# Optimization experiments

Measured on AMD Instinct MI355X. Metric: run time of the kernel, lower is better.

Reference implementation:

```python
import jax, jax.numpy as jnp
import numpy as np

B, L, D = 32, 128, 512
Qn = 16          # n_querys
N, P = 512, 64   # gathered groups x group size


def setup_inputs() -> dict:
    key = jax.random.key(0)
    ks = jax.random.split(key, 10)
    s = 0.02
    return {
        "patch": jax.random.normal(ks[0], (B, L, D), jnp.float32),
        "query": jax.random.normal(ks[1], (1, Qn, D), jnp.float32),
        "Wk": jax.random.normal(ks[2], (D, D), jnp.float32) * s,
        "bk": jnp.zeros((D,), jnp.float32),
        "Wv": jax.random.normal(ks[3], (D, D), jnp.float32) * s,
        "bv": jnp.zeros((D,), jnp.float32),
        "Wf": jax.random.normal(ks[4], (D, 1), jnp.float32) * s,
        "bf": jnp.zeros((1,), jnp.float32),
        "indices": jax.random.randint(ks[5], (N, P), 0, B * L),
        "pos_mask": jax.random.bernoulli(ks[6], 0.8, (N, P)),
    }


def reference(patch, query, Wk, bk, Wv, bv, Wf, bf, indices, pos_mask):
    # patch: [B,L,D]; query: [1,q,D]; indices: [N,P] into B*L; pos_mask: [N,P]
    b, l, d = patch.shape
    q = query.shape[1]
    scale = 1.0 / jnp.sqrt(jnp.asarray(d, patch.dtype))
    Q0 = query[0]                                   # [q,D]
    # Projections (proj_k/proj_v applied to [Q ; patch]); Q row identical across batch
    KQ = Q0 @ Wk + bk                               # [q,D]
    Kp = patch @ Wk + bk                            # [B,L,D]
    VQ = Q0 @ Wv + bv                               # [q,D]
    Vp = patch @ Wv + bv                            # [B,L,D]
    # attn scores: self-token column (same for every batch) + patch columns
    s_self = jnp.einsum('qd,qd->q', Q0, KQ) * scale            # [q]
    s_patch = jnp.einsum('qd,bld->blq', Q0, Kp) * scale        # [B,L,q]
    # gather groups of tokens by flat index
    g = s_patch.reshape(b * l, q)[indices]                     # [N,P,q]
    g = jnp.where(pos_mask[:, :, None], g, -jnp.inf)
    g = jnp.transpose(g, (0, 2, 1))                            # [N,q,P]
    scores = jnp.concatenate(
        [jnp.broadcast_to(s_self[None, :, None], (g.shape[0], q, 1)), g], axis=-1)
    w = jax.nn.softmax(scores, axis=-1)                        # [N,q,P+1]
    # gathered values (value of a token is independent of q in the original)
    Vg = Vp.reshape(b * l, d)[indices]                         # [N,P,D]
    Vg = jnp.where(pos_mask[:, :, None], Vg, 0.0)
    patch_token = w[:, :, 0:1] * VQ[None] \
        + jnp.einsum('nqp,npd->nqd', w[:, :, 1:], Vg)          # [N,q,D]
    # fusion attention pooling over the q query axis
    fw = jax.nn.softmax(jnp.einsum('nqd,do->nqo', patch_token, Wf) + bf, axis=1)
    return jnp.sum(patch_token * fw, axis=1)                   # [N,D]
```

## Files before the change

### kernel.cpp

```cpp
#include <hip/hip_runtime.h>
#include <hip/hip_bf16.h>
#include <math.h>

#define DD    512
#define QN    16
#define NTOK  4096
#define MEXT  4112
#define MPAD  4224
#define NGRP  512
#define PP    64
#define NB    640
#define SCALE 0.04419417382415922f

typedef __bf16 bf16x8 __attribute__((ext_vector_type(8)));
typedef float  f32x4  __attribute__((ext_vector_type(4)));

static __device__ __forceinline__ ushort f2bf(float f) {
    __hip_bfloat16 h = __float2bfloat16(f);
    return *reinterpret_cast<ushort*>(&h);
}

__global__ __launch_bounds__(64) void k1_A(
    const float* __restrict__ query, const float* __restrict__ Wk,
    const float* __restrict__ bk, float* __restrict__ A, float* __restrict__ c0)
{
    const int e = blockIdx.x;
    const int lane = threadIdx.x;
    if (e < DD) {
        float x[8];
#pragma unroll
        for (int j = 0; j < 8; ++j) x[j] = Wk[e * DD + j * 64 + lane];
        for (int q = 0; q < QN; ++q) {
            float s = 0.f;
#pragma unroll
            for (int j = 0; j < 8; ++j) s += x[j] * query[q * DD + j * 64 + lane];
#pragma unroll
            for (int off = 32; off > 0; off >>= 1) s += __shfl_down(s, off, 64);
            if (lane == 0) A[q * DD + e] = s;
        }
    } else {
        const int q = e - DD;
        float s = 0.f;
#pragma unroll
        for (int j = 0; j < 8; ++j)
            s += bk[j * 64 + lane] * query[q * DD + j * 64 + lane];
#pragma unroll
        for (int off = 32; off > 0; off >>= 1) s += __shfl_down(s, off, 64);
        if (lane == 0) c0[q] = s;
    }
}

__global__ __launch_bounds__(256) void k_pack(
    const float* __restrict__ patch, const float* __restrict__ query,
    const float* __restrict__ Wv, const float* __restrict__ Afp,
    ushort* __restrict__ Xb, ushort* __restrict__ Bb)
{
    __shared__ float T[64][65];
    const int b = blockIdx.x;
    const int tid = threadIdx.x;
    if (b < 1056) {
        const int e0 = b * 2048 + tid * 8;
        const int row = e0 >> 9, c = e0 & 511;
        float v[8];
        if (row < NTOK) {
            const float4 a0 = *(const float4*)&patch[(size_t)row * DD + c];
            const float4 a1 = *(const float4*)&patch[(size_t)row * DD + c + 4];
            v[0]=a0.x; v[1]=a0.y; v[2]=a0.z; v[3]=a0.w;
            v[4]=a1.x; v[5]=a1.y; v[6]=a1.z; v[7]=a1.w;
        } else if (row < MEXT) {
            const float4 a0 = *(const float4*)&query[(size_t)(row - NTOK) * DD + c];
            const float4 a1 = *(const float4*)&query[(size_t)(row - NTOK) * DD + c + 4];
            v[0]=a0.x; v[1]=a0.y; v[2]=a0.z; v[3]=a0.w;
            v[4]=a1.x; v[5]=a1.y; v[6]=a1.z; v[7]=a1.w;
        } else {
#pragma unroll
            for (int j = 0; j < 8; ++j) v[j] = 0.f;
        }
        ushort o[8];
#pragma unroll
        for (int j = 0; j < 8; ++j) o[j] = f2bf(v[j]);
        *(uint4*)&Xb[e0] = *(const uint4*)o;
    } else if (b < 1120) {
        const int t = b - 1056;
        const int k0 = (t >> 3) * 64, n0 = (t & 7) * 64;
#pragma unroll
        for (int j = 0; j < 16; ++j) {
            const int idx = tid + j * 256;
            const int r = idx >> 6, c = idx & 63;
            T[r][c] = Wv[(size_t)(k0 + r) * DD + n0 + c];
        }
        __syncthreads();
#pragma unroll
        for (int j = 0; j < 16; ++j) {
            const int idx = tid + j * 256;
            const int r = idx >> 6, c = idx & 63;
            Bb[(size_t)(n0 + r) * DD + k0 + c] = f2bf(T[c][r]);
        }
    } else if (b < 1124) {
        const int e0 = (b - 1120) * 2048 + tid * 8;
        ushort o[8];
#pragma unroll
        for (int j = 0; j < 8; ++j) o[j] = f2bf(Afp[e0 + j]);
        *(uint4*)&Bb[(size_t)DD * DD + e0] = *(const uint4*)o;
    } else {
        const int e0 = (b - 1124) * 2048 + tid * 8;
        *(uint4*)&Bb[(size_t)528 * DD + e0] = make_uint4(0, 0, 0, 0);
    }
}

__global__ __launch_bounds__(256) void k2_mfma(
    const ushort* __restrict__ Xb, const ushort* __restrict__ Bb,
    const float* __restrict__ bv, const float* __restrict__ c0,
    float* __restrict__ Vp, float* __restrict__ S)
{
    __shared__ __align__(16) ushort Xs[128][72];
    __shared__ __align__(16) ushort Bs[128][72];
    const int tid = threadIdx.x;
    const int rowBase = blockIdx.y * 128;
    const int colBase = blockIdx.x * 128;
    const int wave = tid >> 6, lane = tid & 63;
    const int wm = (wave >> 1) * 64, wn = (wave & 1) * 64;
    const int lr = lane & 15;
    const int quad = lane >> 4;

    f32x4 acc[4][4];
    const f32x4 zero = {0.f, 0.f, 0.f, 0.f};
#pragma unroll
    for (int i = 0; i < 4; ++i)
#pragma unroll
        for (int j = 0; j < 4; ++j) acc[i][j] = zero;

    for (int k0 = 0; k0 < DD; k0 += 64) {
#pragma unroll
        for (int i = 0; i < 4; ++i) {
            const int ch = tid + i * 256;
            const int r = ch >> 3, cc = (ch & 7) * 8;
            *(uint4*)&Xs[r][cc] = *(const uint4*)&Xb[(size_t)(rowBase + r) * DD + k0 + cc];
            *(uint4*)&Bs[r][cc] = *(const uint4*)&Bb[(size_t)(colBase + r) * DD + k0 + cc];
        }
        __syncthreads();
#pragma unroll
        for (int kc = 0; kc < 2; ++kc) {
            bf16x8 af[4], bfr[4];
#pragma unroll
            for (int t = 0; t < 4; ++t) {
                af[t]  = *(const bf16x8*)&Xs[wm + t * 16 + lr][kc * 32 + quad * 8];
                bfr[t] = *(const bf16x8*)&Bs[wn + t * 16 + lr][kc * 32 + quad * 8];
            }
#pragma unroll
            for (int mt = 0; mt < 4; ++mt)
#pragma unroll
                for (int nt = 0; nt < 4; ++nt)
                    acc[mt][nt] = __builtin_amdgcn_mfma_f32_16x16x32_bf16(
                        af[mt], bfr[nt], acc[mt][nt], 0, 0, 0);
        }
        __syncthreads();
    }

#pragma unroll
    for (int nt = 0; nt < 4; ++nt) {
        const int col = colBase + wn + nt * 16 + lr;
        const bool isV = (col < DD);
        const bool isS = (col >= DD) && (col < DD + QN);
        const float badd = isV ? bv[col] : (isS ? c0[col - DD] : 0.f);
#pragma unroll
        for (int mt = 0; mt < 4; ++mt) {
#pragma unroll
            for (int r = 0; r < 4; ++r) {
                const int row = rowBase + wm + mt * 16 + quad * 4 + r;
                if (row < MEXT) {
                    const float v = acc[mt][nt][r];
                    if (isV)      Vp[(size_t)row * DD + col] = v + badd;
                    else if (isS) S[row * QN + (col - DD)] = (v + badd) * SCALE;
                }
            }
        }
    }
}

__global__ __launch_bounds__(256) void k4_agg(
    const float* __restrict__ Vp,
    const float* __restrict__ S,
    const int* __restrict__ indices,
    const void* __restrict__ pmask,
    const float* __restrict__ Wf, const float* __restrict__ bf,
    float* __restrict__ out)
{
    __shared__ int   idxs[PP];
    __shared__ int   mval[PP];
    __shared__ int   cidx[PP + 4];
    __shared__ int   cp[PP + 4];
    __shared__ float sc[QN][PP + 2];
    __shared__ float red[QN][4];
    __shared__ float fwq[QN];
    __shared__ int   cntS;

    const int n = blockIdx.x;
    const int tid = threadIdx.x;

    const unsigned int* mw = (const unsigned int*)pmask;
    bool four = true;
#pragma unroll
    for (int i = 0; i < 16; ++i) {
        const unsigned int v = mw[i];
        four = four && (v == 0u || v == 1u || v == 0x3F800000u);
    }

    if (tid < PP) {
        idxs[tid] = indices[n * PP + tid];
        int mv;
        if (four) mv = (mw[n * PP + tid] != 0u);
        else      mv = (((const unsigned char*)pmask)[n * PP + tid] != 0);
        mval[tid] = mv;
        const bool a = (mv != 0);
        const unsigned long long m = __ballot(a);
        const int pos = __popcll(m & ((1ull << tid) - 1ull));
        if (a) { cidx[pos] = idxs[tid]; cp[pos] = tid; }
        if (tid == 0) cntS = (int)__popcll(m);
    }
    __syncthreads();

    for (int e = tid; e < QN * PP; e += 256) {
        const int q = e & (QN - 1), p = e >> 4;
        sc[q][p + 1] = mval[p] ? S[idxs[p] * QN + q] : -INFINITY;
    }
    if (tid < QN) sc[tid][0] = S[(NTOK + tid) * QN + tid];
    __syncthreads();

    if (tid < 4) { cidx[cntS + tid] = 0; cp[cntS + tid] = PP; }
    if (tid < QN) {
        const int q = tid;
        float m = -INFINITY;
        for (int j = 0; j <= PP; ++j) m = fmaxf(m, sc[q][j]);
        float s = 0.f;
        for (int j = 0; j <= PP; ++j) { const float e = __expf(sc[q][j] - m); sc[q][j] = e; s += e; }
        const float inv = 1.f / s;
        for (int j = 0; j <= PP; ++j) sc[q][j] *= inv;
        sc[q][PP + 1] = 0.f;
    }
    __syncthreads();

    const int cnt4 = (cntS + 3) & ~3;
    const int d0 = tid * 2;
    float pt[QN][2];
#pragma unroll
    for (int q = 0; q < QN; ++q) {
        const float w0 = sc[q][0];
        const float2 vq = *(const float2*)&Vp[(size_t)(NTOK + q) * DD + d0];
        pt[q][0] = w0 * vq.x;
        pt[q][1] = w0 * vq.y;
    }
    for (int j0 = 0; j0 < cnt4; j0 += 4) {
        const float2 v0 = *(const float2*)&Vp[(size_t)cidx[j0 + 0] * DD + d0];
        const float2 v1 = *(const float2*)&Vp[(size_t)cidx[j0 + 1] * DD + d0];
        const float2 v2 = *(const float2*)&Vp[(size_t)cidx[j0 + 2] * DD + d0];
        const float2 v3 = *(const float2*)&Vp[(size_t)cidx[j0 + 3] * DD + d0];
        const int p0 = cp[j0], p1 = cp[j0 + 1], p2 = cp[j0 + 2], p3 = cp[j0 + 3];
#pragma unroll
        for (int q = 0; q < QN; ++q) {
            const float w0 = sc[q][p0 + 1], w1 = sc[q][p1 + 1];
            const float w2 = sc[q][p2 + 1], w3 = sc[q][p3 + 1];
            pt[q][0] += w0 * v0.x + w1 * v1.x + w2 * v2.x + w3 * v3.x;
            pt[q][1] += w0 * v0.y + w1 * v1.y + w2 * v2.y + w3 * v3.y;
        }
    }

    const float wf0 = Wf[d0], wf1 = Wf[d0 + 1];
    const int wid = tid >> 6, lane = tid & 63;
#pragma unroll
    for (int q = 0; q < QN; ++q) {
        float s = pt[q][0] * wf0 + pt[q][1] * wf1;
#pragma unroll
        for (int off = 32; off > 0; off >>= 1) s += __shfl_down(s, off, 64);
        if (lane == 0) red[q][wid] = s;
    }
    __syncthreads();
    if (tid == 0) {
        float f[QN];
        float m = -INFINITY;
#pragma unroll
        for (int q = 0; q < QN; ++q) {
            f[q] = red[q][0] + red[q][1] + red[q][2] + red[q][3] + bf[0];
            m = fmaxf(m, f[q]);
        }
        float ssum = 0.f;
#pragma unroll
        for (int q = 0; q < QN; ++q) { f[q] = __expf(f[q] - m); ssum += f[q]; }
        const float inv = 1.f / ssum;
#pragma unroll
        for (int q = 0; q < QN; ++q) fwq[q] = f[q] * inv;
    }
    __syncthreads();

    float o0 = 0.f, o1 = 0.f;
#pragma unroll
    for (int q = 0; q < QN; ++q) {
        const float w = fwq[q];
        o0 += pt[q][0] * w;
        o1 += pt[q][1] * w;
    }
    *(float2*)&out[(size_t)n * DD + d0] = make_float2(o0, o1);
}

extern "C" void kernel_launch(void* const* d_in, const int* in_sizes, int n_in,
                              void* d_out, int out_size, void* d_ws, size_t ws_size,
                              hipStream_t stream)
{
    const float* patch   = (const float*)d_in[0];
    const float* query   = (const float*)d_in[1];
    const float* Wk      = (const float*)d_in[2];
    const float* bk      = (const float*)d_in[3];
    const float* Wv      = (const float*)d_in[4];
    const float* bv      = (const float*)d_in[5];
    const float* Wf      = (const float*)d_in[6];
    const float* bf      = (const float*)d_in[7];
    const int*   indices = (const int*)d_in[8];
    const void*  pmask   = d_in[9];
    float* out = (float*)d_out;

    float* ws = (float*)d_ws;
    float* Vp = ws;
    float* S  = Vp + (size_t)MEXT * DD;
    float* A  = S  + (size_t)MEXT * QN;
    float* c0 = A  + (size_t)QN * DD;
    ushort* Xb = (ushort*)(c0 + 16);
    ushort* Bb = Xb + (size_t)MPAD * DD;

    k1_A   <<<dim3(DD + QN), dim3(64), 0, stream>>>(query, Wk, bk, A, c0);
    k_pack <<<dim3(1152), dim3(256), 0, stream>>>(patch, query, Wv, A, Xb, Bb);
    k2_mfma<<<dim3(5, 33), dim3(256), 0, stream>>>(Xb, Bb, bv, c0, Vp, S);
    k4_agg <<<dim3(NGRP), dim3(256), 0, stream>>>(Vp, S, indices, pmask, Wf, bf, out);
}
```

Baseline: 132.6 us.

## Fuse query-key projection into pack kernel, narrow GEMM tiles, transpose score layout

```diff
diff --git a/kernel.cpp b/kernel.cpp
--- a/kernel.cpp
+++ b/kernel.cpp
@@ -20,40 +20,11 @@
     return *reinterpret_cast<ushort*>(&h);
 }
 
-__global__ __launch_bounds__(64) void k1_A(
-    const float* __restrict__ query, const float* __restrict__ Wk,
-    const float* __restrict__ bk, float* __restrict__ A, float* __restrict__ c0)
-{
-    const int e = blockIdx.x;
-    const int lane = threadIdx.x;
-    if (e < DD) {
-        float x[8];
-#pragma unroll
-        for (int j = 0; j < 8; ++j) x[j] = Wk[e * DD + j * 64 + lane];
-        for (int q = 0; q < QN; ++q) {
-            float s = 0.f;
-#pragma unroll
-            for (int j = 0; j < 8; ++j) s += x[j] * query[q * DD + j * 64 + lane];
-#pragma unroll
-            for (int off = 32; off > 0; off >>= 1) s += __shfl_down(s, off, 64);
-            if (lane == 0) A[q * DD + e] = s;
-        }
-    } else {
-        const int q = e - DD;
-        float s = 0.f;
-#pragma unroll
-        for (int j = 0; j < 8; ++j)
-            s += bk[j * 64 + lane] * query[q * DD + j * 64 + lane];
-#pragma unroll
-        for (int off = 32; off > 0; off >>= 1) s += __shfl_down(s, off, 64);
-        if (lane == 0) c0[q] = s;
-    }
-}
-
-__global__ __launch_bounds__(256) void k_pack(
+__global__ __launch_bounds__(256) void pack_all(
     const float* __restrict__ patch, const float* __restrict__ query,
-    const float* __restrict__ Wv, const float* __restrict__ Afp,
-    ushort* __restrict__ Xb, ushort* __restrict__ Bb)
+    const float* __restrict__ Wv, const float* __restrict__ Wk,
+    const float* __restrict__ bk,
+    ushort* __restrict__ Xb, ushort* __restrict__ Bb, float* __restrict__ c0)
 {
     __shared__ float T[64][65];
     const int b = blockIdx.x;
@@ -96,15 +67,35 @@
             const int r = idx >> 6, c = idx & 63;
             Bb[(size_t)(n0 + r) * DD + k0 + c] = f2bf(T[c][r]);
         }
-    } else if (b < 1124) {
+    } else if (b < 1148) {
         const int e0 = (b - 1120) * 2048 + tid * 8;
-        ushort o[8];
-#pragma unroll
-        for (int j = 0; j < 8; ++j) o[j] = f2bf(Afp[e0 + j]);
-        *(uint4*)&Bb[(size_t)DD * DD + e0] = *(const uint4*)o;
+        *(uint4*)&Bb[(size_t)528 * DD + e0] = make_uint4(0, 0, 0, 0);
     } else {
-        const int e0 = (b - 1124) * 2048 + tid * 8;
-        *(uint4*)&Bb[(size_t)528 * DD + e0] = make_uint4(0, 0, 0, 0);
+        const int wave = tid >> 6, lane = tid & 63;
+        const int g = (b - 1148) * 4 + wave;
+        if (g < DD) {
+            const int e = g;
+            float x[8];
+#pragma unroll
+            for (int j = 0; j < 8; ++j) x[j] = Wk[e * DD + j * 64 + lane];
+            for (int q = 0; q < QN; ++q) {
+                float s = 0.f;
+#pragma unroll
+                for (int j = 0; j < 8; ++j) s += x[j] * query[q * DD + j * 64 + lane];
+#pragma unroll
+                for (int off = 32; off > 0; off >>= 1) s += __shfl_down(s, off, 64);
+                if (lane == 0) Bb[(size_t)(DD + q) * DD + e] = f2bf(s);
+            }
+        } else {
+            const int q = g - DD;
+            float s = 0.f;
+#pragma unroll
+            for (int j = 0; j < 8; ++j)
+                s += bk[j * 64 + lane] * query[q * DD + j * 64 + lane];
+#pragma unroll
+            for (int off = 32; off > 0; off >>= 1) s += __shfl_down(s, off, 64);
+            if (lane == 0) c0[q] = s;
+        }
     }
 }
 
@@ -114,21 +105,19 @@
     float* __restrict__ Vp, float* __restrict__ S)
 {
     __shared__ __align__(16) ushort Xs[128][72];
-    __shared__ __align__(16) ushort Bs[128][72];
+    __shared__ __align__(16) ushort Bs[64][72];
     const int tid = threadIdx.x;
     const int rowBase = blockIdx.y * 128;
-    const int colBase = blockIdx.x * 128;
+    const int colBase = blockIdx.x * 64;
     const int wave = tid >> 6, lane = tid & 63;
-    const int wm = (wave >> 1) * 64, wn = (wave & 1) * 64;
+    const int wm = (wave >> 1) * 64, wn = (wave & 1) * 32;
     const int lr = lane & 15;
     const int quad = lane >> 4;
 
-    f32x4 acc[4][4];
+    f32x4 acc[4][2];
     const f32x4 zero = {0.f, 0.f, 0.f, 0.f};
 #pragma unroll
-    for (int i = 0; i < 4; ++i)
-#pragma unroll
-        for (int j = 0; j < 4; ++j) acc[i][j] = zero;
+    for (int i = 0; i < 4; ++i) { acc[i][0] = zero; acc[i][1] = zero; }
 
     for (int k0 = 0; k0 < DD; k0 += 64) {
 #pragma unroll
@@ -136,21 +125,27 @@
             const int ch = tid + i * 256;
             const int r = ch >> 3, cc = (ch & 7) * 8;
             *(uint4*)&Xs[r][cc] = *(const uint4*)&Xb[(size_t)(rowBase + r) * DD + k0 + cc];
+        }
+#pragma unroll
+        for (int i = 0; i < 2; ++i) {
+            const int ch = tid + i * 256;
+            const int r = ch >> 3, cc = (ch & 7) * 8;
             *(uint4*)&Bs[r][cc] = *(const uint4*)&Bb[(size_t)(colBase + r) * DD + k0 + cc];
         }
         __syncthreads();
 #pragma unroll
         for (int kc = 0; kc < 2; ++kc) {
-            bf16x8 af[4], bfr[4];
-#pragma unroll
-            for (int t = 0; t < 4; ++t) {
-                af[t]  = *(const bf16x8*)&Xs[wm + t * 16 + lr][kc * 32 + quad * 8];
-                bfr[t] = *(const bf16x8*)&Bs[wn + t * 16 + lr][kc * 32 + quad * 8];
-            }
+            bf16x8 af[4], bfr[2];
+#pragma unroll
+            for (int t = 0; t < 4; ++t)
+                af[t] = *(const bf16x8*)&Xs[wm + t * 16 + lr][kc * 32 + quad * 8];
+#pragma unroll
+            for (int u = 0; u < 2; ++u)
+                bfr[u] = *(const bf16x8*)&Bs[wn + u * 16 + lr][kc * 32 + quad * 8];
 #pragma unroll
             for (int mt = 0; mt < 4; ++mt)
 #pragma unroll
-                for (int nt = 0; nt < 4; ++nt)
+                for (int nt = 0; nt < 2; ++nt)
                     acc[mt][nt] = __builtin_amdgcn_mfma_f32_16x16x32_bf16(
                         af[mt], bfr[nt], acc[mt][nt], 0, 0, 0);
         }
@@ -158,7 +153,7 @@
     }
 
 #pragma unroll
-    for (int nt = 0; nt < 4; ++nt) {
+    for (int nt = 0; nt < 2; ++nt) {
         const int col = colBase + wn + nt * 16 + lr;
         const bool isV = (col < DD);
         const bool isS = (col >= DD) && (col < DD + QN);
@@ -190,7 +185,7 @@
     __shared__ int   mval[PP];
     __shared__ int   cidx[PP + 4];
     __shared__ int   cp[PP + 4];
-    __shared__ float sc[QN][PP + 2];
+    __shared__ float scT[PP + 2][QN];
     __shared__ float red[QN][4];
     __shared__ float fwq[QN];
     __shared__ int   cntS;
@@ -221,22 +216,22 @@
     __syncthreads();
 
     for (int e = tid; e < QN * PP; e += 256) {
-        const int q = e & (QN - 1), p = e >> 4;
-        sc[q][p + 1] = mval[p] ? S[idxs[p] * QN + q] : -INFINITY;
-    }
-    if (tid < QN) sc[tid][0] = S[(NTOK + tid) * QN + tid];
+        const int p = e >> 4, q = e & 15;
+        scT[p + 1][q] = mval[p] ? S[idxs[p] * QN + q] : -INFINITY;
+    }
+    if (tid < QN) scT[0][tid] = S[(NTOK + tid) * QN + tid];
     __syncthreads();
 
     if (tid < 4) { cidx[cntS + tid] = 0; cp[cntS + tid] = PP; }
     if (tid < QN) {
         const int q = tid;
         float m = -INFINITY;
-        for (int j = 0; j <= PP; ++j) m = fmaxf(m, sc[q][j]);
+        for (int j = 0; j <= PP; ++j) m = fmaxf(m, scT[j][q]);
         float s = 0.f;
-        for (int j = 0; j <= PP; ++j) { const float e = __expf(sc[q][j] - m); sc[q][j] = e; s += e; }
+        for (int j = 0; j <= PP; ++j) { const float e = __expf(scT[j][q] - m); scT[j][q] = e; s += e; }
         const float inv = 1.f / s;
-        for (int j = 0; j <= PP; ++j) sc[q][j] *= inv;
-        sc[q][PP + 1] = 0.f;
+        for (int j = 0; j <= PP; ++j) scT[j][q] *= inv;
+        scT[PP + 1][q] = 0.f;
     }
     __syncthreads();
 
@@ -245,23 +240,41 @@
     float pt[QN][2];
 #pragma unroll
     for (int q = 0; q < QN; ++q) {
-        const float w0 = sc[q][0];
+        const float w0 = scT[0][q];
         const float2 vq = *(const float2*)&Vp[(size_t)(NTOK + q) * DD + d0];
         pt[q][0] = w0 * vq.x;
         pt[q][1] = w0 * vq.y;
     }
     for (int j0 = 0; j0 < cnt4; j0 += 4) {
-        const float2 v0 = *(const float2*)&Vp[(size_t)cidx[j0 + 0] * DD + d0];
-        const float2 v1 = *(const float2*)&Vp[(size_t)cidx[j0 + 1] * DD + d0];
-        const float2 v2 = *(const float2*)&Vp[(size_t)cidx[j0 + 2] * DD + d0];
-        const float2 v3 = *(const float2*)&Vp[(size_t)cidx[j0 + 3] * DD + d0];
-        const int p0 = cp[j0], p1 = cp[j0 + 1], p2 = cp[j0 + 2], p3 = cp[j0 + 3];
-#pragma unroll
-        for (int q = 0; q < QN; ++q) {
-            const float w0 = sc[q][p0 + 1], w1 = sc[q][p1 + 1];
-            const float w2 = sc[q][p2 + 1], w3 = sc[q][p3 + 1];
-            pt[q][0] += w0 * v0.x + w1 * v1.x + w2 * v2.x + w3 * v3.x;
-            pt[q][1] += w0 * v0.y + w1 * v1.y + w2 * v2.y + w3 * v3.y;
+        float2 v[4]; int p[4];
+#pragma unroll
+        for (int pi = 0; pi < 4; ++pi) {
+            v[pi] = *(const float2*)&Vp[(size_t)cidx[j0 + pi] * DD + d0];
+            p[pi] = cp[j0 + pi] + 1;
+        }
+#pragma unroll
+        for (int pi = 0; pi < 4; ++pi) {
+            const float4 wa = *(const float4*)&scT[p[pi]][0];
+            const float4 wb = *(const float4*)&scT[p[pi]][4];
+            const float4 wc = *(const float4*)&scT[p[pi]][8];
+            const float4 wd = *(const float4*)&scT[p[pi]][12];
+            const float vx = v[pi].x, vy = v[pi].y;
+            pt[ 0][0] += wa.x*vx; pt[ 0][1] += wa.x*vy;
+            pt[ 1][0] += wa.y*vx; pt[ 1][1] += wa.y*vy;
+            pt[ 2][0] += wa.z*vx; pt[ 2][1] += wa.z*vy;
+            pt[ 3][0] += wa.w*vx; pt[ 3][1] += wa.w*vy;
+            pt[ 4][0] += wb.x*vx; pt[ 4][1] += wb.x*vy;
+            pt[ 5][0] += wb.y*vx; pt[ 5][1] += wb.y*vy;
+            pt[ 6][0] += wb.z*vx; pt[ 6][1] += wb.z*vy;
+            pt[ 7][0] += wb.w*vx; pt[ 7][1] += wb.w*vy;
+            pt[ 8][0] += wc.x*vx; pt[ 8][1] += wc.x*vy;
+            pt[ 9][0] += wc.y*vx; pt[ 9][1] += wc.y*vy;
+            pt[10][0] += wc.z*vx; pt[10][1] += wc.z*vy;
+            pt[11][0] += wc.w*vx; pt[11][1] += wc.w*vy;
+            pt[12][0] += wd.x*vx; pt[12][1] += wd.x*vy;
+            pt[13][0] += wd.y*vx; pt[13][1] += wd.y*vy;
+            pt[14][0] += wd.z*vx; pt[14][1] += wd.z*vy;
+            pt[15][0] += wd.w*vx; pt[15][1] += wd.w*vy;
         }
     }
 
@@ -321,13 +334,11 @@
     float* ws = (float*)d_ws;
     float* Vp = ws;
     float* S  = Vp + (size_t)MEXT * DD;
-    float* A  = S  + (size_t)MEXT * QN;
-    float* c0 = A  + (size_t)QN * DD;
+    float* c0 = S  + (size_t)MEXT * QN;
     ushort* Xb = (ushort*)(c0 + 16);
     ushort* Bb = Xb + (size_t)MPAD * DD;
 
-    k1_A   <<<dim3(DD + QN), dim3(64), 0, stream>>>(query, Wk, bk, A, c0);
-    k_pack <<<dim3(1152), dim3(256), 0, stream>>>(patch, query, Wv, A, Xb, Bb);
-    k2_mfma<<<dim3(5, 33), dim3(256), 0, stream>>>(Xb, Bb, bv, c0, Vp, S);
-    k4_agg <<<dim3(NGRP), dim3(256), 0, stream>>>(Vp, S, indices, pmask, Wf, bf, out);
-}
+    pack_all<<<dim3(1280), dim3(256), 0, stream>>>(patch, query, Wv, Wk, bk, Xb, Bb, c0);
+    k2_mfma <<<dim3(10, 33), dim3(256), 0, stream>>>(Xb, Bb, bv, c0, Vp, S);
+    k4_agg  <<<dim3(NGRP), dim3(256), 0, stream>>>(Vp, S, indices, pmask, Wf, bf, out);
+}
```

Result: faster. 124.0 us (-6.5%).
